# Performance work log

Hardware: AMD Instinct MI355X
Metric: run time of the kernel (lower is better)

## Reference

```python
import jax, jax.numpy as jnp
import numpy as np

B, L, D, T = 8, 4096, 2048, 128  # batch, seq len, hidden dim, max num targets
LN_EPS = 1e-5


def setup_inputs() -> dict:
    key = jax.random.key(0)
    ks = jax.random.split(key, 6)
    context_repr = jax.random.normal(ks[0], (B, L, D), dtype=jnp.float32)
    # varying target counts per row, max exactly T (so num_targets == T as in torch)
    counts = np.minimum((np.arange(B) * 41 + 7) % (T + 1), T)
    counts[0] = T
    counts = jnp.asarray(counts, dtype=jnp.int32)
    pos = jnp.arange(L)
    target_mask = (pos[None, :] < counts[:, None]).astype(jnp.float32)  # [B,L]
    context_mask = 1.0 - target_mask  # valid context = non-target positions
    s1 = 1.0 / np.sqrt(D)
    s2 = 1.0 / np.sqrt(2 * D)
    W1 = jax.random.uniform(ks[1], (D, 2 * D), jnp.float32, -s1, s1)
    b1 = jax.random.uniform(ks[2], (2 * D,), jnp.float32, -s1, s1)
    gamma = jnp.ones((2 * D,), jnp.float32)
    beta = jnp.zeros((2 * D,), jnp.float32)
    W2 = jax.random.uniform(ks[3], (2 * D, D), jnp.float32, -s2, s2)
    b2 = jax.random.uniform(ks[4], (D,), jnp.float32, -s2, s2)
    return {
        "context_repr": context_repr,
        "target_mask": target_mask,
        "context_mask": context_mask,
        "W1": W1, "b1": b1, "gamma": gamma, "beta": beta, "W2": W2, "b2": b2,
        "num_targets": T,
    }


def reference(context_repr, target_mask, context_mask, W1, b1, gamma, beta, W2, b2, num_targets):
    # masked mean pool: sum over ALL positions (targets assumed zeroed),
    # divide by number of valid context positions (faithful to torch code)
    ctx_count = context_mask.sum(axis=-1)                     # [B]
    ctx_sum = context_repr.sum(axis=1)                        # [B,D]
    mean = ctx_sum / jnp.maximum(ctx_count, 1.0)[:, None]
    mean = jnp.where((ctx_count > 0)[:, None], mean, 0.0)     # [B,D]
    # MLP: Linear -> GELU(exact) -> LayerNorm -> Linear
    h = jax.nn.gelu(mean @ W1 + b1, approximate=False)        # [B,2D]
    mu = h.mean(axis=-1, keepdims=True)
    var = jnp.mean((h - mu) ** 2, axis=-1, keepdims=True)
    hn = (h - mu) * jax.lax.rsqrt(var + LN_EPS) * gamma + beta
    out = hn @ W2 + b2                                        # [B,D]
    # scatter prediction into first num_tgt slots per row, rest zeros
    tgt_counts = target_mask.sum(axis=-1)                     # [B]
    valid = jnp.arange(num_targets)[None, :] < tgt_counts[:, None]  # [B,T]
    return jnp.where(valid[:, :, None], out[:, None, :], 0.0)  # [B,T,D]
```

## Files before the change

kernel.cpp:

```cpp
#include <hip/hip_runtime.h>
#include <math.h>

#define B_    8
#define L_    4096
#define D_    2048
#define D2_   4096
#define T_    128
#define LN_EPS_ 1e-5f

#define LCHUNK 128
#define KC1    64
#define KC2    64

__global__ void k_masks(const float* __restrict__ tmask,
                        const float* __restrict__ cmask,
                        float* __restrict__ cnt, float* __restrict__ tcnt) {
  const int b = blockIdx.x;
  const int tid = threadIdx.x;
  float sc = 0.f, st = 0.f;
  for (int i = tid; i < L_; i += 256) {
    sc += cmask[b * L_ + i];
    st += tmask[b * L_ + i];
  }
  __shared__ float sC[256], sT[256];
  sC[tid] = sc; sT[tid] = st;
  __syncthreads();
  for (int off = 128; off > 0; off >>= 1) {
    if (tid < off) { sC[tid] += sC[tid + off]; sT[tid] += sT[tid + off]; }
    __syncthreads();
  }
  if (tid == 0) { cnt[b] = sC[0]; tcnt[b] = sT[0]; }
}

__global__ void k_pool(const float* __restrict__ x, float* __restrict__ csum) {
  const int lc = blockIdx.x;
  const int db = blockIdx.y;
  const int b  = blockIdx.z;
  const int d  = db * 1024 + threadIdx.x * 4;
  const float* p = x + (size_t)b * L_ * D_ + (size_t)lc * LCHUNK * D_ + d;
  float ax = 0.f, ay = 0.f, az = 0.f, aw = 0.f;
  #pragma unroll 8
  for (int l = 0; l < LCHUNK; ++l) {
    const float4 v = *reinterpret_cast<const float4*>(p + (size_t)l * D_);
    ax += v.x; ay += v.y; az += v.z; aw += v.w;
  }
  float* o = csum + b * D_ + d;
  atomicAdd(o + 0, ax); atomicAdd(o + 1, ay);
  atomicAdd(o + 2, az); atomicAdd(o + 3, aw);
}

__global__ void k_gemv1(const float* __restrict__ S,
                        const float* __restrict__ W1,
                        float* __restrict__ h_pre) {
  const int j  = blockIdx.x * 256 + threadIdx.x;
  const int k0 = blockIdx.y * KC1;
  __shared__ float s[B_][KC1];
  for (int i = threadIdx.x; i < B_ * KC1; i += 256) {
    const int bb = i / KC1, kk = i % KC1;
    s[bb][kk] = S[bb * D_ + k0 + kk];
  }
  __syncthreads();
  float acc[B_];
  #pragma unroll
  for (int bb = 0; bb < B_; ++bb) acc[bb] = 0.f;
  const float* w = W1 + (size_t)k0 * D2_ + j;
  #pragma unroll 4
  for (int k = 0; k < KC1; ++k) {
    const float wv = w[(size_t)k * D2_];
    #pragma unroll
    for (int bb = 0; bb < B_; ++bb) acc[bb] += s[bb][k] * wv;
  }
  #pragma unroll
  for (int bb = 0; bb < B_; ++bb) atomicAdd(&h_pre[bb * D2_ + j], acc[bb]);
}

__global__ void k_gelu_ln(const float* __restrict__ h_pre,
                          const float* __restrict__ cnt,
                          const float* __restrict__ b1,
                          const float* __restrict__ gamma,
                          const float* __restrict__ beta,
                          float* __restrict__ hn) {
  const int b = blockIdx.x;
  const int tid = threadIdx.x;
  const float c = cnt[b];
  const float scale = (c > 0.f) ? (1.f / fmaxf(c, 1.f)) : 0.f;
  const int j = tid * 4;
  float4 hp = *reinterpret_cast<const float4*>(h_pre + (size_t)b * D2_ + j);
  float4 bb = *reinterpret_cast<const float4*>(b1 + j);
  float g[4];
  {
    const float v0 = hp.x * scale + bb.x;
    const float v1 = hp.y * scale + bb.y;
    const float v2 = hp.z * scale + bb.z;
    const float v3 = hp.w * scale + bb.w;
    g[0] = 0.5f * v0 * (1.f + erff(v0 * 0.70710678118654752f));
    g[1] = 0.5f * v1 * (1.f + erff(v1 * 0.70710678118654752f));
    g[2] = 0.5f * v2 * (1.f + erff(v2 * 0.70710678118654752f));
    g[3] = 0.5f * v3 * (1.f + erff(v3 * 0.70710678118654752f));
  }
  float lsum = g[0] + g[1] + g[2] + g[3];
  float lsq  = g[0]*g[0] + g[1]*g[1] + g[2]*g[2] + g[3]*g[3];
  __shared__ float sS[1024], sQ[1024];
  sS[tid] = lsum; sQ[tid] = lsq;
  __syncthreads();
  for (int off = 512; off > 0; off >>= 1) {
    if (tid < off) { sS[tid] += sS[tid + off]; sQ[tid] += sQ[tid + off]; }
    __syncthreads();
  }
  const float mu  = sS[0] * (1.f / D2_);
  const float var = sQ[0] * (1.f / D2_) - mu * mu;
  const float rs  = rsqrtf(var + LN_EPS_);
  float4 gm = *reinterpret_cast<const float4*>(gamma + j);
  float4 bt = *reinterpret_cast<const float4*>(beta + j);
  float4 o;
  o.x = (g[0] - mu) * rs * gm.x + bt.x;
  o.y = (g[1] - mu) * rs * gm.y + bt.y;
  o.z = (g[2] - mu) * rs * gm.z + bt.z;
  o.w = (g[3] - mu) * rs * gm.w + bt.w;
  *reinterpret_cast<float4*>(hn + (size_t)b * D2_ + j) = o;
}

__global__ void k_gemv2(const float* __restrict__ HN,
                        const float* __restrict__ W2,
                        float* __restrict__ out_pre) {
  const int d  = blockIdx.x * 256 + threadIdx.x;
  const int j0 = blockIdx.y * KC2;
  __shared__ float s[B_][KC2];
  for (int i = threadIdx.x; i < B_ * KC2; i += 256) {
    const int bb = i / KC2, jj = i % KC2;
    s[bb][jj] = HN[bb * D2_ + j0 + jj];
  }
  __syncthreads();
  float acc[B_];
  #pragma unroll
  for (int bb = 0; bb < B_; ++bb) acc[bb] = 0.f;
  const float* w = W2 + (size_t)j0 * D_ + d;
  #pragma unroll 4
  for (int k = 0; k < KC2; ++k) {
    const float wv = w[(size_t)k * D_];
    #pragma unroll
    for (int bb = 0; bb < B_; ++bb) acc[bb] += s[bb][k] * wv;
  }
  #pragma unroll
  for (int bb = 0; bb < B_; ++bb) atomicAdd(&out_pre[bb * D_ + d], acc[bb]);
}

__global__ void k_scatter(const float* __restrict__ out_pre,
                          const float* __restrict__ b2,
                          const float* __restrict__ tcnt,
                          float* __restrict__ out) {
  const size_t idx = ((size_t)blockIdx.x * 256 + threadIdx.x) * 4;
  const int d  = (int)(idx % D_);
  const int bt = (int)(idx / D_);
  const int t  = bt % T_;
  const int b  = bt / T_;
  float4 v = make_float4(0.f, 0.f, 0.f, 0.f);
  if (t < (int)(tcnt[b] + 0.5f)) {
    const float4 op = *reinterpret_cast<const float4*>(out_pre + b * D_ + d);
    const float4 bv = *reinterpret_cast<const float4*>(b2 + d);
    v = make_float4(op.x + bv.x, op.y + bv.y, op.z + bv.z, op.w + bv.w);
  }
  *reinterpret_cast<float4*>(out + idx) = v;
}

extern "C" void kernel_launch(void* const* d_in, const int* in_sizes, int n_in,
                              void* d_out, int out_size, void* d_ws, size_t ws_size,
                              hipStream_t stream) {
  const float* context_repr = (const float*)d_in[0];
  const float* target_mask  = (const float*)d_in[1];
  const float* context_mask = (const float*)d_in[2];
  const float* W1    = (const float*)d_in[3];
  const float* b1    = (const float*)d_in[4];
  const float* gamma = (const float*)d_in[5];
  const float* beta  = (const float*)d_in[6];
  const float* W2    = (const float*)d_in[7];
  const float* b2    = (const float*)d_in[8];
  float* out = (float*)d_out;

  float* ws       = (float*)d_ws;
  float* ctx_sum  = ws;
  float* cnt      = ctx_sum + B_ * D_;
  float* tcnt     = cnt + B_;
  float* h_pre    = tcnt + B_;
  float* hn       = h_pre + B_ * D2_;
  float* out_pre  = hn + B_ * D2_;
  const size_t ws_used = (size_t)(B_*D_ + 2*B_ + 2*B_*D2_ + B_*D_) * sizeof(float);

  hipMemsetAsync(d_ws, 0, ws_used, stream);

  k_masks<<<dim3(B_), dim3(256), 0, stream>>>(target_mask, context_mask, cnt, tcnt);

  k_pool<<<dim3(L_ / LCHUNK, D_ / 1024, B_), dim3(256), 0, stream>>>(context_repr, ctx_sum);

  k_gemv1<<<dim3(D2_ / 256, D_ / KC1), dim3(256), 0, stream>>>(ctx_sum, W1, h_pre);

  k_gelu_ln<<<dim3(B_), dim3(1024), 0, stream>>>(h_pre, cnt, b1, gamma, beta, hn);

  k_gemv2<<<dim3(D_ / 256, D2_ / KC2), dim3(256), 0, stream>>>(hn, W2, out_pre);

  const int n_out4 = out_size / 4;
  k_scatter<<<dim3((n_out4 + 255) / 256), dim3(256), 0, stream>>>(out_pre, b2, tcnt, out);
}
```

Measured before the change: 439.6 us.

## Replace atomic accumulation with partial-sum buffers and deterministic reductions

Every atomicAdd into the pooled sums and the two GEMV outputs becomes a write into per-chunk partial buffers. The consumer kernels then reduce those buffers: gemv1 sums the pool partials, gelu_ln sums the gemv1 partials, and a new reduce kernel adds b2. This drops the workspace memset and the atomic contention, and it vectorises the mask reads. The cost is extra partial-buffer traffic: 32 pool partials are reread per gemv1 block, plus 32×B×4096 partials in gelu_ln, which runs on only 8 blocks.

```diff
diff --git a/kernel.cpp b/kernel.cpp
--- a/kernel.cpp
+++ b/kernel.cpp
@@ -8,9 +8,12 @@
 #define T_    128
 #define LN_EPS_ 1e-5f
 
-#define LCHUNK 128
+#define NLC    32
+#define LCHUNK (L_ / NLC)
 #define KC1    64
+#define NK1    (D_ / KC1)
 #define KC2    64
+#define NK2    (D2_ / KC2)
 
 __global__ void k_masks(const float* __restrict__ tmask,
                         const float* __restrict__ cmask,
@@ -18,9 +21,11 @@
   const int b = blockIdx.x;
   const int tid = threadIdx.x;
   float sc = 0.f, st = 0.f;
-  for (int i = tid; i < L_; i += 256) {
-    sc += cmask[b * L_ + i];
-    st += tmask[b * L_ + i];
+  for (int i = tid * 4; i < L_; i += 256 * 4) {
+    const float4 c4 = *reinterpret_cast<const float4*>(cmask + b * L_ + i);
+    const float4 t4 = *reinterpret_cast<const float4*>(tmask + b * L_ + i);
+    sc += c4.x + c4.y + c4.z + c4.w;
+    st += t4.x + t4.y + t4.z + t4.w;
   }
   __shared__ float sC[256], sT[256];
   sC[tid] = sc; sT[tid] = st;
@@ -32,32 +37,36 @@
   if (tid == 0) { cnt[b] = sC[0]; tcnt[b] = sT[0]; }
 }
 
-__global__ void k_pool(const float* __restrict__ x, float* __restrict__ csum) {
+__global__ void k_pool(const float* __restrict__ x, float* __restrict__ part) {
   const int lc = blockIdx.x;
   const int db = blockIdx.y;
   const int b  = blockIdx.z;
   const int d  = db * 1024 + threadIdx.x * 4;
   const float* p = x + (size_t)b * L_ * D_ + (size_t)lc * LCHUNK * D_ + d;
   float ax = 0.f, ay = 0.f, az = 0.f, aw = 0.f;
-  #pragma unroll 8
+  #pragma unroll 16
   for (int l = 0; l < LCHUNK; ++l) {
     const float4 v = *reinterpret_cast<const float4*>(p + (size_t)l * D_);
     ax += v.x; ay += v.y; az += v.z; aw += v.w;
   }
-  float* o = csum + b * D_ + d;
-  atomicAdd(o + 0, ax); atomicAdd(o + 1, ay);
-  atomicAdd(o + 2, az); atomicAdd(o + 3, aw);
-}
-
-__global__ void k_gemv1(const float* __restrict__ S,
+  float4 o = make_float4(ax, ay, az, aw);
+  *reinterpret_cast<float4*>(part + ((size_t)lc * B_ + b) * D_ + d) = o;
+}
+
+__global__ void k_gemv1(const float* __restrict__ part_pool,
                         const float* __restrict__ W1,
-                        float* __restrict__ h_pre) {
+                        float* __restrict__ part1) {
   const int j  = blockIdx.x * 256 + threadIdx.x;
-  const int k0 = blockIdx.y * KC1;
+  const int ky = blockIdx.y;
+  const int k0 = ky * KC1;
   __shared__ float s[B_][KC1];
   for (int i = threadIdx.x; i < B_ * KC1; i += 256) {
     const int bb = i / KC1, kk = i % KC1;
-    s[bb][kk] = S[bb * D_ + k0 + kk];
+    float v = 0.f;
+    #pragma unroll 8
+    for (int lc = 0; lc < NLC; ++lc)
+      v += part_pool[((size_t)lc * B_ + bb) * D_ + k0 + kk];
+    s[bb][kk] = v;
   }
   __syncthreads();
   float acc[B_];
@@ -71,10 +80,11 @@
     for (int bb = 0; bb < B_; ++bb) acc[bb] += s[bb][k] * wv;
   }
   #pragma unroll
-  for (int bb = 0; bb < B_; ++bb) atomicAdd(&h_pre[bb * D2_ + j], acc[bb]);
-}
-
-__global__ void k_gelu_ln(const float* __restrict__ h_pre,
+  for (int bb = 0; bb < B_; ++bb)
+    part1[((size_t)ky * B_ + bb) * D2_ + j] = acc[bb];
+}
+
+__global__ void k_gelu_ln(const float* __restrict__ part1,
                           const float* __restrict__ cnt,
                           const float* __restrict__ b1,
                           const float* __restrict__ gamma,
@@ -85,14 +95,20 @@
   const float c = cnt[b];
   const float scale = (c > 0.f) ? (1.f / fmaxf(c, 1.f)) : 0.f;
   const int j = tid * 4;
-  float4 hp = *reinterpret_cast<const float4*>(h_pre + (size_t)b * D2_ + j);
-  float4 bb = *reinterpret_cast<const float4*>(b1 + j);
+  float hx = 0.f, hy = 0.f, hz = 0.f, hw = 0.f;
+  #pragma unroll 8
+  for (int ky = 0; ky < NK1; ++ky) {
+    const float4 v = *reinterpret_cast<const float4*>(
+        part1 + ((size_t)ky * B_ + b) * D2_ + j);
+    hx += v.x; hy += v.y; hz += v.z; hw += v.w;
+  }
+  const float4 bb = *reinterpret_cast<const float4*>(b1 + j);
   float g[4];
   {
-    const float v0 = hp.x * scale + bb.x;
-    const float v1 = hp.y * scale + bb.y;
-    const float v2 = hp.z * scale + bb.z;
-    const float v3 = hp.w * scale + bb.w;
+    const float v0 = hx * scale + bb.x;
+    const float v1 = hy * scale + bb.y;
+    const float v2 = hz * scale + bb.z;
+    const float v3 = hw * scale + bb.w;
     g[0] = 0.5f * v0 * (1.f + erff(v0 * 0.70710678118654752f));
     g[1] = 0.5f * v1 * (1.f + erff(v1 * 0.70710678118654752f));
     g[2] = 0.5f * v2 * (1.f + erff(v2 * 0.70710678118654752f));
@@ -110,8 +126,8 @@
   const float mu  = sS[0] * (1.f / D2_);
   const float var = sQ[0] * (1.f / D2_) - mu * mu;
   const float rs  = rsqrtf(var + LN_EPS_);
-  float4 gm = *reinterpret_cast<const float4*>(gamma + j);
-  float4 bt = *reinterpret_cast<const float4*>(beta + j);
+  const float4 gm = *reinterpret_cast<const float4*>(gamma + j);
+  const float4 bt = *reinterpret_cast<const float4*>(beta + j);
   float4 o;
   o.x = (g[0] - mu) * rs * gm.x + bt.x;
   o.y = (g[1] - mu) * rs * gm.y + bt.y;
@@ -122,9 +138,10 @@
 
 __global__ void k_gemv2(const float* __restrict__ HN,
                         const float* __restrict__ W2,
-                        float* __restrict__ out_pre) {
+                        float* __restrict__ part2) {
   const int d  = blockIdx.x * 256 + threadIdx.x;
-  const int j0 = blockIdx.y * KC2;
+  const int ky = blockIdx.y;
+  const int j0 = ky * KC2;
   __shared__ float s[B_][KC2];
   for (int i = threadIdx.x; i < B_ * KC2; i += 256) {
     const int bb = i / KC2, jj = i % KC2;
@@ -142,11 +159,29 @@
     for (int bb = 0; bb < B_; ++bb) acc[bb] += s[bb][k] * wv;
   }
   #pragma unroll
-  for (int bb = 0; bb < B_; ++bb) atomicAdd(&out_pre[bb * D_ + d], acc[bb]);
+  for (int bb = 0; bb < B_; ++bb)
+    part2[((size_t)ky * B_ + bb) * D_ + d] = acc[bb];
+}
+
+__global__ void k_reduce2(const float* __restrict__ part2,
+                          const float* __restrict__ b2,
+                          float* __restrict__ out_pre) {
+  const int idx = (blockIdx.x * 256 + threadIdx.x) * 4;
+  const int b = idx / D_;
+  const int d = idx % D_;
+  float ax = 0.f, ay = 0.f, az = 0.f, aw = 0.f;
+  #pragma unroll 8
+  for (int ky = 0; ky < NK2; ++ky) {
+    const float4 v = *reinterpret_cast<const float4*>(
+        part2 + ((size_t)ky * B_ + b) * D_ + d);
+    ax += v.x; ay += v.y; az += v.z; aw += v.w;
+  }
+  const float4 bv = *reinterpret_cast<const float4*>(b2 + d);
+  *reinterpret_cast<float4*>(out_pre + idx) =
+      make_float4(ax + bv.x, ay + bv.y, az + bv.z, aw + bv.w);
 }
 
 __global__ void k_scatter(const float* __restrict__ out_pre,
-                          const float* __restrict__ b2,
                           const float* __restrict__ tcnt,
                           float* __restrict__ out) {
   const size_t idx = ((size_t)blockIdx.x * 256 + threadIdx.x) * 4;
@@ -156,9 +191,7 @@
   const int b  = bt / T_;
   float4 v = make_float4(0.f, 0.f, 0.f, 0.f);
   if (t < (int)(tcnt[b] + 0.5f)) {
-    const float4 op = *reinterpret_cast<const float4*>(out_pre + b * D_ + d);
-    const float4 bv = *reinterpret_cast<const float4*>(b2 + d);
-    v = make_float4(op.x + bv.x, op.y + bv.y, op.z + bv.z, op.w + bv.w);
+    v = *reinterpret_cast<const float4*>(out_pre + b * D_ + d);
   }
   *reinterpret_cast<float4*>(out + idx) = v;
 }
@@ -177,27 +210,27 @@
   const float* b2    = (const float*)d_in[8];
   float* out = (float*)d_out;
 
-  float* ws       = (float*)d_ws;
-  float* ctx_sum  = ws;
-  float* cnt      = ctx_sum + B_ * D_;
-  float* tcnt     = cnt + B_;
-  float* h_pre    = tcnt + B_;
-  float* hn       = h_pre + B_ * D2_;
-  float* out_pre  = hn + B_ * D2_;
-  const size_t ws_used = (size_t)(B_*D_ + 2*B_ + 2*B_*D2_ + B_*D_) * sizeof(float);
-
-  hipMemsetAsync(d_ws, 0, ws_used, stream);
+  float* ws        = (float*)d_ws;
+  float* part_pool = ws;
+  float* cnt       = part_pool + (size_t)NLC * B_ * D_;
+  float* tcnt      = cnt + B_;
+  float* part1     = tcnt + B_;
+  float* hn        = part1 + (size_t)NK1 * B_ * D2_;
+  float* part2     = hn + (size_t)B_ * D2_;
+  float* out_pre   = part2 + (size_t)NK2 * B_ * D_;
 
   k_masks<<<dim3(B_), dim3(256), 0, stream>>>(target_mask, context_mask, cnt, tcnt);
 
-  k_pool<<<dim3(L_ / LCHUNK, D_ / 1024, B_), dim3(256), 0, stream>>>(context_repr, ctx_sum);
-
-  k_gemv1<<<dim3(D2_ / 256, D_ / KC1), dim3(256), 0, stream>>>(ctx_sum, W1, h_pre);
-
-  k_gelu_ln<<<dim3(B_), dim3(1024), 0, stream>>>(h_pre, cnt, b1, gamma, beta, hn);
-
-  k_gemv2<<<dim3(D_ / 256, D2_ / KC2), dim3(256), 0, stream>>>(hn, W2, out_pre);
+  k_pool<<<dim3(NLC, 2, B_), dim3(256), 0, stream>>>(context_repr, part_pool);
+
+  k_gemv1<<<dim3(D2_ / 256, NK1), dim3(256), 0, stream>>>(part_pool, W1, part1);
+
+  k_gelu_ln<<<dim3(B_), dim3(1024), 0, stream>>>(part1, cnt, b1, gamma, beta, hn);
+
+  k_gemv2<<<dim3(D_ / 256, NK2), dim3(256), 0, stream>>>(hn, W2, part2);
+
+  k_reduce2<<<dim3((B_ * D_) / 1024), dim3(256), 0, stream>>>(part2, b2, out_pre);
 
   const int n_out4 = out_size / 4;
-  k_scatter<<<dim3((n_out4 + 255) / 256), dim3(256), 0, stream>>>(out_pre, b2, tcnt, out);
-}
+  k_scatter<<<dim3((n_out4 + 255) / 256), dim3(256), 0, stream>>>(out_pre, tcnt, out);
+}
```

New measurement: 447.2 us. Within noise of the previous version (+1.7%).
